# Kernel tuning notes

Measured on AMD Instinct MI355X. Metric: run time of the kernel, lower is better.

## Reference

```python
import jax, jax.numpy as jnp
import numpy as np

B, S, D = 32, 2048, 1024
TEMP = 9.0  # RelaxedBernoulli temperature (torch.tensor([9]))


def setup_inputs() -> dict:
    key = jax.random.key(0)
    ks = jax.random.split(key, 12)
    sd = 1.0 / np.sqrt(D)
    sd2 = 1.0 / np.sqrt(2 * D)
    return {
        "h_t": jax.random.normal(ks[0], (B, D), jnp.float32),
        "h_s": jax.random.normal(ks[1], (B, S, D), jnp.float32),
        "auxi_hs": jax.random.normal(ks[2], (B, S, D), jnp.float32),
        "noise_u": jax.random.uniform(ks[3], (B, S, 1), jnp.float32),
        # linear_map: Linear(2*dim, 1) with bias
        "Wmap": jax.random.normal(ks[4], (2 * D,), jnp.float32) * sd2,
        "bmap": jax.random.normal(ks[5], (), jnp.float32) * sd2,
        # mlp_h: Linear(dim, dim) + Tanh + Linear(dim, 1)
        "W1": jax.random.normal(ks[6], (D, D), jnp.float32) * sd,
        "b1": jax.random.normal(ks[7], (D,), jnp.float32) * sd,
        "W2": jax.random.normal(ks[8], (D,), jnp.float32) * sd,
        "b2": jax.random.normal(ks[9], (), jnp.float32) * sd,
        # linear_out: Linear(2*dim, dim, bias=False) (attn_type='dot')
        "Wout": jax.random.normal(ks[10], (D, 2 * D), jnp.float32) * sd2,
    }


def reference(h_t, h_s, auxi_hs, noise_u, Wmap, bmap, W1, b1, W2, b2, Wout):
    # h_t: (B, D) one-step query; h_s, auxi_hs: (B, S, D)
    d = h_s.shape[-1]
    # linear_map(concat(auxi_hs, H_t)) without materializing the (B,S,2D) concat
    Wm_a, Wm_t = Wmap[:d], Wmap[d:]
    logits_p = jnp.einsum('bsd,d->bs', auxi_hs, Wm_a) + (h_t @ Wm_t)[:, None] + bmap  # (B,S)
    logits_p = logits_p[..., None]  # (B,S,1); note logit(sigmoid(x)) == x
    # RelaxedBernoulli(temp=9, probs=sigmoid(logits_p)).sample() with explicit uniform noise
    eps = 1e-7
    u = jnp.clip(noise_u, eps, 1.0 - eps)
    logistic = jnp.log(u) - jnp.log1p(-u)  # (B,S,1)
    G = jax.nn.sigmoid((logits_p + logistic) / TEMP)  # (B,S,1)
    # mlp_h(h_s): Linear -> tanh -> Linear
    e = jnp.einsum('bsd,d->bs', jnp.tanh(jnp.einsum('bsd,ed->bse', h_s, W1) + b1), W2) + b2
    e = e[..., None]  # (B,S,1)
    # custom softmax: max over dim 0 (batch!), exp, gate
    v = jnp.max(e, axis=0, keepdims=True)  # (1,S,1)
    scores = jnp.exp(e - v) * G  # (B,S,1)
    align = scores[..., 0] / jnp.sum(scores[..., 0], axis=1, keepdims=True)  # (B,S)
    c = jnp.einsum('bs,bsd->bd', align, h_s)  # (B,D)
    attn_h = jnp.tanh(jnp.concatenate([c, h_t], axis=-1) @ Wout.T)  # (B,D)
    return attn_h, align
```

## Files before the change

### kernel.cpp

```cpp
#include <hip/hip_runtime.h>
#include <hip/hip_bf16.h>
#include <math.h>

#define B_ 32
#define S_ 2048
#define D_ 1024
#define TEMP_ 9.0f

typedef __attribute__((ext_vector_type(8))) short short8;
typedef __attribute__((ext_vector_type(4))) float f32x4;
typedef __attribute__((ext_vector_type(4))) unsigned short ushort4v;

__device__ __forceinline__ unsigned short f2b(float f) {
  union { float f; unsigned int u; } v; v.f = f;
  unsigned int r = v.u;
  r += 0x7fffu + ((r >> 16) & 1u);
  return (unsigned short)(r >> 16);
}
__device__ __forceinline__ float b2f(unsigned short b) {
  union { float f; unsigned int u; } v; v.u = ((unsigned int)b) << 16;
  return v.f;
}
__device__ __forceinline__ float tanh_fast(float x) {
  float ez = __expf(2.f * x);
  return 1.f - __fdividef(2.f, ez + 1.f);
}

#define GLOAD_LDS16(g, l) \
  __builtin_amdgcn_global_load_lds((const __attribute__((address_space(1))) void*)(g), \
                                   (__attribute__((address_space(3))) void*)(l), 16, 0, 0)

__global__ void k_conv(const float* __restrict__ src, unsigned short* __restrict__ dst, int n8) {
  int i = blockIdx.x * 256 + threadIdx.x;
  if (i >= n8) return;
  const float4* g = reinterpret_cast<const float4*>(src) + (size_t)i * 2;
  float4 x0 = g[0], x1 = g[1];
  uint4 w;
  w.x = f2b(x0.x) | ((unsigned)f2b(x0.y) << 16);
  w.y = f2b(x0.z) | ((unsigned)f2b(x0.w) << 16);
  w.z = f2b(x1.x) | ((unsigned)f2b(x1.y) << 16);
  w.w = f2b(x1.z) | ((unsigned)f2b(x1.w) << 16);
  reinterpret_cast<uint4*>(dst)[i] = w;
}

__global__ void k_pack_w1(const float* __restrict__ W1, unsigned short* __restrict__ w1t) {
  int c2 = blockIdx.x * 256 + threadIdx.x;
  int l   = c2 & 63;
  int n   = (c2 >> 6) & 7;
  int T   = (c2 >> 9) & 31;
  int rid = c2 >> 14;
  int col = (rid >> 1) * 256 + (rid & 1) * 128 + n * 16 + (l & 15);
  int k0  = T * 32 + (l >> 4) * 8;
  const float* src = W1 + (size_t)col * D_ + k0;
  float4 x0 = *reinterpret_cast<const float4*>(src);
  float4 x1 = *reinterpret_cast<const float4*>(src + 4);
  uint4 w;
  w.x = f2b(x0.x) | ((unsigned)f2b(x0.y) << 16);
  w.y = f2b(x0.z) | ((unsigned)f2b(x0.w) << 16);
  w.z = f2b(x1.x) | ((unsigned)f2b(x1.y) << 16);
  w.w = f2b(x1.z) | ((unsigned)f2b(x1.w) << 16);
  reinterpret_cast<uint4*>(w1t)[c2] = w;
}

__global__ void k0_tdot(const float* __restrict__ h_t, const float* __restrict__ Wmap,
                        const float* __restrict__ bmap, float* __restrict__ tdot) {
  int b = blockIdx.x;
  int t = threadIdx.x;
  float p = 0.f;
  for (int k = t; k < D_; k += 256) p += h_t[b*D_ + k] * Wmap[D_ + k];
  __shared__ float red[256];
  red[t] = p; __syncthreads();
  for (int off = 128; off > 0; off >>= 1) { if (t < off) red[t] += red[t+off]; __syncthreads(); }
  if (t == 0) tdot[b] = red[0] + bmap[0];
}

__global__ void k1_gate(const float* __restrict__ aux, const float* __restrict__ Wmap,
                        const float* __restrict__ noise, const float* __restrict__ tdot,
                        float* __restrict__ Gout) {
  int w = (blockIdx.x * 256 + threadIdx.x) >> 6;
  int lane = threadIdx.x & 63;
  const float4* arow = reinterpret_cast<const float4*>(aux + (size_t)w * D_);
  const float4* wrow = reinterpret_cast<const float4*>(Wmap);
  float p = 0.f;
  for (int it = 0; it < 4; ++it) {
    float4 a = arow[it*64 + lane];
    float4 m = wrow[it*64 + lane];
    p += a.x*m.x + a.y*m.y + a.z*m.z + a.w*m.w;
  }
  for (int msk = 32; msk > 0; msk >>= 1) p += __shfl_xor(p, msk);
  if (lane == 0) {
    int b = w >> 11;
    float logits = p + tdot[b];
    float u = noise[w];
    u = fminf(fmaxf(u, 1e-7f), 1.f - 1e-7f);
    float logistic = logf(u) - log1pf(-u);
    float x = (logits + logistic) / TEMP_;
    Gout[w] = 1.f / (1.f + expf(-x));
  }
}

extern __shared__ unsigned short lds2[];

__global__ __launch_bounds__(256, 2) void k2gt(
    const unsigned short* __restrict__ Ag, const unsigned short* __restrict__ w1t,
    const float* __restrict__ b1, const float* __restrict__ W2,
    float* __restrict__ e_buf,
    const float* __restrict__ aux, const float* __restrict__ Wmap,
    const float* __restrict__ noise, const float* __restrict__ tdot,
    float* __restrict__ Gout) {
  int bid = blockIdx.x;
  int xcd = bid & 7;
  int sub = bid >> 3;
  int cc  = sub & 3;
  int rc  = xcd + 8 * (sub >> 2);
  int rowBase = rc * 128;
  int colBase = cc * 256;

  int t = threadIdx.x;
  int lane = t & 63;
  int wv = t >> 6;
  int wr = wv >> 1, wc = wv & 1;
  int kslot = lane >> 4;

  int aOff[4];
#pragma unroll
  for (int m = 0; m < 4; ++m) {
    int r = wr * 64 + m * 16 + (lane & 15);
    aOff[m] = r * 64 + ((kslot ^ ((r >> 1) & 3)) << 4);
  }

  const unsigned short* gA[2];
  int dstA[2];
#pragma unroll
  for (int i = 0; i < 2; ++i) {
    int c = i * 256 + t;
    int r = c >> 2;
    int clog = (c & 3) ^ ((r >> 1) & 3);
    gA[i] = Ag + (size_t)(rowBase + r) * D_ + clog * 8;
    dstA[i] = c * 16;
  }

  const unsigned short* pBbase = w1t + (size_t)(cc * 2 + wc) * 131072 + lane * 8;

  f32x4 acc[4][8] = {};
  short8 bfA[8], bfB[8];

#define STAGE(TT) do {                                                         \
    char* _ba = (char*)lds2 + ((TT) & 3) * 8192;                               \
    GLOAD_LDS16(gA[0] + (TT) * 32, _ba + dstA[0]);                             \
    GLOAD_LDS16(gA[1] + (TT) * 32, _ba + dstA[1]);                             \
  } while (0)

#define K2_TILE(T, VM, DO_B, DO_S, BFC, BFN) do {                              \
    asm volatile("s_waitcnt lgkmcnt(0)\n\ts_waitcnt vmcnt(" #VM ")" ::: "memory"); \
    __builtin_amdgcn_s_barrier();                                              \
    const char* _ab = (const char*)lds2 + ((T) & 3) * 8192;                    \
    short8 af[4];                                                              \
    _Pragma("unroll")                                                          \
    for (int m = 0; m < 4; ++m)                                                \
      af[m] = *reinterpret_cast<const short8*>(_ab + aOff[m]);                 \
    if (DO_B) {                                                                \
      _Pragma("unroll")                                                        \
      for (int n = 0; n < 8; ++n)                                              \
        BFN[n] = *reinterpret_cast<const short8*>(pBbase + ((T) + 1) * 4096 + n * 512); \
    }                                                                          \
    if (DO_S) STAGE((T) + 3);                                                  \
    __builtin_amdgcn_s_setprio(1);                                             \
    _Pragma("unroll")                                                          \
    for (int m = 0; m < 4; ++m)                                                \
      _Pragma("unroll")                                                        \
      for (int n = 0; n < 8; ++n)                                              \
        acc[m][n] = __builtin_amdgcn_mfma_f32_16x16x32_bf16(af[m], BFC[n], acc[m][n], 0, 0, 0); \
    __builtin_amdgcn_s_setprio(0);                                             \
  } while (0)

  STAGE(0); STAGE(1); STAGE(2);
#pragma unroll
  for (int n = 0; n < 8; ++n)
    bfA[n] = *reinterpret_cast<const short8*>(pBbase + n * 512);

  K2_TILE(0, 0, true, true, bfA, bfB);
#pragma unroll
  for (int tt = 1; tt < 28; tt += 2) {
    K2_TILE(tt,     2, true, true, bfB, bfA);
    K2_TILE(tt + 1, 2, true, true, bfA, bfB);
  }
  K2_TILE(29, 2, true,  false, bfB, bfA);
  K2_TILE(30, 0, true,  false, bfA, bfB);
  K2_TILE(31, 0, false, false, bfB, bfA);
#undef K2_TILE
#undef STAGE

  float b1v[8], w2v[8];
#pragma unroll
  for (int n = 0; n < 8; ++n) {
    int col = colBase + wc * 128 + n * 16 + (lane & 15);
    b1v[n] = b1[col];
    w2v[n] = W2[col];
  }
#pragma unroll
  for (int m = 0; m < 4; ++m) {
#pragma unroll
    for (int j = 0; j < 4; ++j) {
      float s = 0.f;
#pragma unroll
      for (int n = 0; n < 8; ++n)
        s += tanh_fast(acc[m][n][j] + b1v[n]) * w2v[n];
      s += __shfl_xor(s, 1);
      s += __shfl_xor(s, 2);
      s += __shfl_xor(s, 4);
      s += __shfl_xor(s, 8);
      if ((lane & 15) == 0) {
        int row = rowBase + wr * 64 + m * 16 + ((lane >> 4) << 2) + j;
        atomicAdd(&e_buf[row], s);
      }
    }
  }

  {
    const float4* wrow = reinterpret_cast<const float4*>(Wmap);
    float4 m0 = wrow[lane], m1 = wrow[64 + lane], m2 = wrow[128 + lane], m3 = wrow[192 + lane];
    int rowG = (bid << 5) | (wv << 3);
#pragma unroll 2
    for (int i = 0; i < 8; ++i) {
      int row = rowG + i;
      const float4* arow = reinterpret_cast<const float4*>(aux + (size_t)row * D_);
      float4 a0 = arow[lane], a1 = arow[64 + lane], a2 = arow[128 + lane], a3 = arow[192 + lane];
      float p = a0.x*m0.x + a0.y*m0.y + a0.z*m0.z + a0.w*m0.w
              + a1.x*m1.x + a1.y*m1.y + a1.z*m1.z + a1.w*m1.w
              + a2.x*m2.x + a2.y*m2.y + a2.z*m2.z + a2.w*m2.w
              + a3.x*m3.x + a3.y*m3.y + a3.z*m3.z + a3.w*m3.w;
      for (int msk = 32; msk > 0; msk >>= 1) p += __shfl_xor(p, msk);
      if (lane == 0) {
        float logits = p + tdot[row >> 11];
        float u = noise[row];
        u = fminf(fmaxf(u, 1e-7f), 1.f - 1e-7f);
        float logistic = logf(u) - log1pf(-u);
        float x = (logits + logistic) / TEMP_;
        Gout[row] = 1.f / (1.f + expf(-x));
      }
    }
  }
}

#define BM 128
#define BN 128
#define BK 64
__global__ __launch_bounds__(256) void k2_egemm_f32(
    const float* __restrict__ h_s, const float* __restrict__ W1,
    const float* __restrict__ b1, const float* __restrict__ W2,
    float* __restrict__ e_buf) {
  __shared__ unsigned short As[BM * BK];
  __shared__ unsigned short Bs[BN * BK];
  int bid = blockIdx.x;
  int colBase = (bid & 7) * BN;
  int rowBase = (bid >> 3) * BM;
  int t = threadIdx.x;
  int lane = t & 63;
  int wave = t >> 6;
  int wr = wave >> 1, wc = wave & 1;
  f32x4 acc[4][4] = {};
  for (int k0 = 0; k0 < D_; k0 += BK) {
    __syncthreads();
    for (int i = 0; i < 4; ++i) {
      int flat = i*256 + t;
      int r = flat >> 3;
      int c8 = flat & 7;
      int byte = (r*128 + c8*16) ^ ((r & 7) << 4);
      {
        const float4* g = reinterpret_cast<const float4*>(h_s + (size_t)(rowBase + r)*D_ + k0 + c8*8);
        float4 x0 = g[0], x1 = g[1];
        uint4 w;
        w.x = f2b(x0.x) | ((unsigned)f2b(x0.y) << 16);
        w.y = f2b(x0.z) | ((unsigned)f2b(x0.w) << 16);
        w.z = f2b(x1.x) | ((unsigned)f2b(x1.y) << 16);
        w.w = f2b(x1.z) | ((unsigned)f2b(x1.w) << 16);
        *reinterpret_cast<uint4*>(reinterpret_cast<char*>(As) + byte) = w;
      }
      {
        const float4* g = reinterpret_cast<const float4*>(W1 + (size_t)(colBase + r)*D_ + k0 + c8*8);
        float4 x0 = g[0], x1 = g[1];
        uint4 w;
        w.x = f2b(x0.x) | ((unsigned)f2b(x0.y) << 16);
        w.y = f2b(x0.z) | ((unsigned)f2b(x0.w) << 16);
        w.z = f2b(x1.x) | ((unsigned)f2b(x1.y) << 16);
        w.w = f2b(x1.z) | ((unsigned)f2b(x1.w) << 16);
        *reinterpret_cast<uint4*>(reinterpret_cast<char*>(Bs) + byte) = w;
      }
    }
    __syncthreads();
    for (int kk = 0; kk < BK; kk += 32) {
      short8 af[4], bf[4];
      int kByte = kk*2 + ((lane >> 4) << 4);
      for (int m = 0; m < 4; ++m) {
        int r = wr*64 + m*16 + (lane & 15);
        int byte = (r*128 + kByte) ^ ((r & 7) << 4);
        af[m] = *reinterpret_cast<const short8*>(reinterpret_cast<const char*>(As) + byte);
      }
      for (int n = 0; n < 4; ++n) {
        int r = wc*64 + n*16 + (lane & 15);
        int byte = (r*128 + kByte) ^ ((r & 7) << 4);
        bf[n] = *reinterpret_cast<const short8*>(reinterpret_cast<const char*>(Bs) + byte);
      }
      for (int m = 0; m < 4; ++m)
        for (int n = 0; n < 4; ++n)
          acc[m][n] = __builtin_amdgcn_mfma_f32_16x16x32_bf16(af[m], bf[n], acc[m][n], 0, 0, 0);
    }
  }
  float b1v[4], w2v[4];
  for (int n = 0; n < 4; ++n) {
    int col = colBase + wc*64 + n*16 + (lane & 15);
    b1v[n] = b1[col];
    w2v[n] = W2[col];
  }
  for (int m = 0; m < 4; ++m) {
    for (int j = 0; j < 4; ++j) {
      float s = 0.f;
      for (int n = 0; n < 4; ++n)
        s += tanhf(acc[m][n][j] + b1v[n]) * w2v[n];
      s += __shfl_xor(s, 1);
      s += __shfl_xor(s, 2);
      s += __shfl_xor(s, 4);
      s += __shfl_xor(s, 8);
      if ((lane & 15) == 0) {
        int row = rowBase + wr*64 + m*16 + ((lane >> 4) << 2) + j;
        atomicAdd(&e_buf[row], s);
      }
    }
  }
}

__global__ void k3a_vmax(const float* __restrict__ e_buf, float* __restrict__ v) {
  int s = blockIdx.x * 256 + threadIdx.x;
  if (s >= S_) return;
  float m = -1e30f;
  for (int b = 0; b < B_; ++b) m = fmaxf(m, e_buf[b*S_ + s]);
  v[s] = m;
}

__global__ void k3b_align(const float* __restrict__ e_buf, const float* __restrict__ v,
                          float* __restrict__ galign) {
  int b = blockIdx.x;
  int t = threadIdx.x;
  __shared__ float sc[S_];
  __shared__ float red[256];
  float p = 0.f;
  for (int s = t; s < S_; s += 256) {
    float x = expf(e_buf[b*S_ + s] - v[s]) * galign[b*S_ + s];
    sc[s] = x;
    p += x;
  }
  red[t] = p; __syncthreads();
  for (int off = 128; off > 0; off >>= 1) { if (t < off) red[t] += red[t+off]; __syncthreads(); }
  float inv = 1.f / red[0];
  for (int s = t; s < S_; s += 256) galign[b*S_ + s] = sc[s] * inv;
}

__global__ void k4_ctx_bf16(const unsigned short* __restrict__ hsb, const float* __restrict__ align,
                            float* __restrict__ c) {
  int bid = blockIdx.x;
  int b = bid >> 6;
  int sBase = (bid & 63) * 32;
  int t = threadIdx.x;
  float4 accv = {0.f, 0.f, 0.f, 0.f};
  for (int si = 0; si < 32; ++si) {
    int s = sBase + si;
    float a = align[b*S_ + s];
    ushort4v hv = *reinterpret_cast<const ushort4v*>(hsb + (size_t)(b*S_ + s)*D_ + t*4);
    accv.x += a*b2f(hv.x); accv.y += a*b2f(hv.y); accv.z += a*b2f(hv.z); accv.w += a*b2f(hv.w);
  }
  atomicAdd(&c[b*D_ + t*4 + 0], accv.x);
  atomicAdd(&c[b*D_ + t*4 + 1], accv.y);
  atomicAdd(&c[b*D_ + t*4 + 2], accv.z);
  atomicAdd(&c[b*D_ + t*4 + 3], accv.w);
}

__global__ void k4_ctx_f32(const float* __restrict__ h_s, const float* __restrict__ align,
                           float* __restrict__ c) {
  int bid = blockIdx.x;
  int b = bid >> 6;
  int sBase = (bid & 63) * 32;
  int t = threadIdx.x;
  float4 accv = {0.f, 0.f, 0.f, 0.f};
  for (int si = 0; si < 32; ++si) {
    int s = sBase + si;
    float a = align[b*S_ + s];
    float4 hv = *reinterpret_cast<const float4*>(h_s + (size_t)(b*S_ + s)*D_ + t*4);
    accv.x += a*hv.x; accv.y += a*hv.y; accv.z += a*hv.z; accv.w += a*hv.w;
  }
  atomicAdd(&c[b*D_ + t*4 + 0], accv.x);
  atomicAdd(&c[b*D_ + t*4 + 1], accv.y);
  atomicAdd(&c[b*D_ + t*4 + 2], accv.z);
  atomicAdd(&c[b*D_ + t*4 + 3], accv.w);
}

__global__ void k5_out(const float* __restrict__ c, const float* __restrict__ h_t,
                       const float* __restrict__ Wout, float* __restrict__ out) {
  int W = (blockIdx.x * 256 + threadIdx.x) >> 6;
  int lane = threadIdx.x & 63;
  int b = W >> 10;
  int o = W & 1023;
  const float* wrow = Wout + (size_t)o * (2 * D_);
  float p = 0.f;
  for (int it = 0; it < 16; ++it) {
    int k = it*64 + lane;
    p += c[b*D_ + k] * wrow[k];
  }
  for (int it = 16; it < 32; ++it) {
    int k = it*64 + lane;
    p += h_t[b*D_ + (k - D_)] * wrow[k];
  }
  for (int m = 32; m > 0; m >>= 1) p += __shfl_xor(p, m);
  if (lane == 0) out[b*D_ + o] = tanhf(p);
}

extern "C" void kernel_launch(void* const* d_in, const int* in_sizes, int n_in,
                              void* d_out, int out_size, void* d_ws, size_t ws_size,
                              hipStream_t stream) {
  const float* h_t   = (const float*)d_in[0];
  const float* h_s   = (const float*)d_in[1];
  const float* aux   = (const float*)d_in[2];
  const float* noise = (const float*)d_in[3];
  const float* Wmap  = (const float*)d_in[4];
  const float* bmap  = (const float*)d_in[5];
  const float* W1    = (const float*)d_in[6];
  const float* b1    = (const float*)d_in[7];
  const float* W2    = (const float*)d_in[8];
  const float* Wout  = (const float*)d_in[10];

  float* out    = (float*)d_out;
  float* galign = out + B_*D_;

  const size_t HS_N   = (size_t)B_*S_*D_;
  const size_t W1_N   = (size_t)D_*D_;
  const size_t needed = HS_N*2 + W1_N*2 + (65536 + 32 + 2048 + 32768) * sizeof(float);

  if (ws_size >= needed) {
    unsigned short* hs_bf = (unsigned short*)d_ws;
    unsigned short* w1t   = hs_bf + HS_N;
    float* fws   = (float*)(w1t + W1_N);
    float* e_buf = fws;
    float* tdot  = fws + 65536;
    float* v     = fws + 65568;
    float* c     = fws + 67616;

    hipMemsetAsync(e_buf, 0, 65536 * sizeof(float), stream);
    hipMemsetAsync(c, 0, 32768 * sizeof(float), stream);

    hipFuncSetAttribute(reinterpret_cast<const void*>(k2gt),
                        hipFuncAttributeMaxDynamicSharedMemorySize, 32768);

    k_conv<<<(int)(HS_N/8/256), 256, 0, stream>>>(h_s, hs_bf, (int)(HS_N/8));
    k_pack_w1<<<512, 256, 0, stream>>>(W1, w1t);
    k0_tdot<<<32, 256, 0, stream>>>(h_t, Wmap, bmap, tdot);
    k2gt<<<2048, 256, 32768, stream>>>(hs_bf, w1t, b1, W2, e_buf,
                                       aux, Wmap, noise, tdot, galign);
    k3a_vmax<<<8, 256, 0, stream>>>(e_buf, v);
    k3b_align<<<32, 256, 0, stream>>>(e_buf, v, galign);
    k4_ctx_bf16<<<2048, 256, 0, stream>>>(hs_bf, galign, c);
    k5_out<<<8192, 256, 0, stream>>>(c, h_t, Wout, out);
  } else {
    float* ws    = (float*)d_ws;
    float* e_buf = ws;
    float* tdot  = ws + 65536;
    float* v     = ws + 65568;
    float* c     = ws + 67616;

    hipMemsetAsync(e_buf, 0, 65536 * sizeof(float), stream);
    hipMemsetAsync(c, 0, 32768 * sizeof(float), stream);

    k0_tdot<<<32, 256, 0, stream>>>(h_t, Wmap, bmap, tdot);
    k1_gate<<<16384, 256, 0, stream>>>(aux, Wmap, noise, tdot, galign);
    k2_egemm_f32<<<4096, 256, 0, stream>>>(h_s, W1, b1, W2, e_buf);
    k3a_vmax<<<8, 256, 0, stream>>>(e_buf, v);
    k3b_align<<<32, 256, 0, stream>>>(e_buf, v, galign);
    k4_ctx_f32<<<2048, 256, 0, stream>>>(h_s, galign, c);
    k5_out<<<8192, 256, 0, stream>>>(c, h_t, Wout, out);
  }
}
```

Baseline: 350.0 us.

## Fuse h_s fp32-to-bf16 conversion into GEMM tile loads, drop separate conversion pass

```diff
diff --git a/kernel.cpp b/kernel.cpp
--- a/kernel.cpp
+++ b/kernel.cpp
@@ -21,6 +21,11 @@
   union { float f; unsigned int u; } v; v.u = ((unsigned int)b) << 16;
   return v.f;
 }
+__device__ __forceinline__ unsigned cvtpk(float a, float b) {
+  unsigned r;
+  asm("v_cvt_pk_bf16_f32 %0, %1, %2" : "=v"(r) : "v"(a), "v"(b));
+  return r;
+}
 __device__ __forceinline__ float tanh_fast(float x) {
   float ez = __expf(2.f * x);
   return 1.f - __fdividef(2.f, ez + 1.f);
@@ -29,19 +34,6 @@
 #define GLOAD_LDS16(g, l) \
   __builtin_amdgcn_global_load_lds((const __attribute__((address_space(1))) void*)(g), \
                                    (__attribute__((address_space(3))) void*)(l), 16, 0, 0)
-
-__global__ void k_conv(const float* __restrict__ src, unsigned short* __restrict__ dst, int n8) {
-  int i = blockIdx.x * 256 + threadIdx.x;
-  if (i >= n8) return;
-  const float4* g = reinterpret_cast<const float4*>(src) + (size_t)i * 2;
-  float4 x0 = g[0], x1 = g[1];
-  uint4 w;
-  w.x = f2b(x0.x) | ((unsigned)f2b(x0.y) << 16);
-  w.y = f2b(x0.z) | ((unsigned)f2b(x0.w) << 16);
-  w.z = f2b(x1.x) | ((unsigned)f2b(x1.y) << 16);
-  w.w = f2b(x1.z) | ((unsigned)f2b(x1.w) << 16);
-  reinterpret_cast<uint4*>(dst)[i] = w;
-}
 
 __global__ void k_pack_w1(const float* __restrict__ W1, unsigned short* __restrict__ w1t) {
   int c2 = blockIdx.x * 256 + threadIdx.x;
@@ -101,8 +93,8 @@
 
 extern __shared__ unsigned short lds2[];
 
-__global__ __launch_bounds__(256, 2) void k2gt(
-    const unsigned short* __restrict__ Ag, const unsigned short* __restrict__ w1t,
+__global__ __launch_bounds__(256, 2) void k2f(
+    const float* __restrict__ h_s, const unsigned short* __restrict__ w1t,
     const float* __restrict__ b1, const float* __restrict__ W2,
     float* __restrict__ e_buf,
     const float* __restrict__ aux, const float* __restrict__ Wmap,
@@ -122,21 +114,22 @@
   int wr = wv >> 1, wc = wv & 1;
   int kslot = lane >> 4;
 
-  int aOff[4];
+  int aOff0[4], aOff1[4];
 #pragma unroll
   for (int m = 0; m < 4; ++m) {
     int r = wr * 64 + m * 16 + (lane & 15);
-    aOff[m] = r * 64 + ((kslot ^ ((r >> 1) & 3)) << 4);
-  }
-
-  const unsigned short* gA[2];
-  int dstA[2];
-#pragma unroll
-  for (int i = 0; i < 2; ++i) {
+    aOff0[m] = r * 128 + (((2 * kslot)     ^ (r & 7)) << 4);
+    aOff1[m] = r * 128 + (((2 * kslot + 1) ^ (r & 7)) << 4);
+  }
+
+  const float* gA[4];
+  int dstA[4];
+#pragma unroll
+  for (int i = 0; i < 4; ++i) {
     int c = i * 256 + t;
-    int r = c >> 2;
-    int clog = (c & 3) ^ ((r >> 1) & 3);
-    gA[i] = Ag + (size_t)(rowBase + r) * D_ + clog * 8;
+    int r = c >> 3;
+    int lg = (c & 7) ^ (r & 7);
+    gA[i] = h_s + (size_t)(rowBase + r) * D_ + lg * 4;
     dstA[i] = c * 16;
   }
 
@@ -146,25 +139,39 @@
   short8 bfA[8], bfB[8];
 
 #define STAGE(TT) do {                                                         \
-    char* _ba = (char*)lds2 + ((TT) & 3) * 8192;                               \
+    char* _ba = (char*)lds2 + ((TT) & 3) * 16384;                              \
     GLOAD_LDS16(gA[0] + (TT) * 32, _ba + dstA[0]);                             \
     GLOAD_LDS16(gA[1] + (TT) * 32, _ba + dstA[1]);                             \
+    GLOAD_LDS16(gA[2] + (TT) * 32, _ba + dstA[2]);                             \
+    GLOAD_LDS16(gA[3] + (TT) * 32, _ba + dstA[3]);                             \
   } while (0)
 
 #define K2_TILE(T, VM, DO_B, DO_S, BFC, BFN) do {                              \
     asm volatile("s_waitcnt lgkmcnt(0)\n\ts_waitcnt vmcnt(" #VM ")" ::: "memory"); \
     __builtin_amdgcn_s_barrier();                                              \
-    const char* _ab = (const char*)lds2 + ((T) & 3) * 8192;                    \
-    short8 af[4];                                                              \
+    const char* _ab = (const char*)lds2 + ((T) & 3) * 16384;                   \
+    f32x4 lo[4], hi[4];                                                        \
     _Pragma("unroll")                                                          \
-    for (int m = 0; m < 4; ++m)                                                \
-      af[m] = *reinterpret_cast<const short8*>(_ab + aOff[m]);                 \
+    for (int m = 0; m < 4; ++m) {                                              \
+      lo[m] = *reinterpret_cast<const f32x4*>(_ab + aOff0[m]);                 \
+      hi[m] = *reinterpret_cast<const f32x4*>(_ab + aOff1[m]);                 \
+    }                                                                          \
     if (DO_B) {                                                                \
       _Pragma("unroll")                                                        \
       for (int n = 0; n < 8; ++n)                                              \
         BFN[n] = *reinterpret_cast<const short8*>(pBbase + ((T) + 1) * 4096 + n * 512); \
     }                                                                          \
     if (DO_S) STAGE((T) + 3);                                                  \
+    short8 af[4];                                                              \
+    _Pragma("unroll")                                                          \
+    for (int m = 0; m < 4; ++m) {                                              \
+      union { unsigned u[4]; short8 s; } cv;                                   \
+      cv.u[0] = cvtpk(lo[m][0], lo[m][1]);                                     \
+      cv.u[1] = cvtpk(lo[m][2], lo[m][3]);                                     \
+      cv.u[2] = cvtpk(hi[m][0], hi[m][1]);                                     \
+      cv.u[3] = cvtpk(hi[m][2], hi[m][3]);                                     \
+      af[m] = cv.s;                                                            \
+    }                                                                          \
     __builtin_amdgcn_s_setprio(1);                                             \
     _Pragma("unroll")                                                          \
     for (int m = 0; m < 4; ++m)                                                \
@@ -181,11 +188,11 @@
 
   K2_TILE(0, 0, true, true, bfA, bfB);
 #pragma unroll
-  for (int tt = 1; tt < 28; tt += 2) {
-    K2_TILE(tt,     2, true, true, bfB, bfA);
-    K2_TILE(tt + 1, 2, true, true, bfA, bfB);
-  }
-  K2_TILE(29, 2, true,  false, bfB, bfA);
+  for (int tt = 1; tt < 29; tt += 2) {
+    K2_TILE(tt,     4, true, true, bfB, bfA);
+    K2_TILE(tt + 1, 4, true, true, bfA, bfB);
+  }
+  K2_TILE(29, 4, true,  false, bfB, bfA);
   K2_TILE(30, 0, true,  false, bfA, bfB);
   K2_TILE(31, 0, false, false, bfB, bfA);
 #undef K2_TILE
@@ -356,25 +363,6 @@
   for (int s = t; s < S_; s += 256) galign[b*S_ + s] = sc[s] * inv;
 }
 
-__global__ void k4_ctx_bf16(const unsigned short* __restrict__ hsb, const float* __restrict__ align,
-                            float* __restrict__ c) {
-  int bid = blockIdx.x;
-  int b = bid >> 6;
-  int sBase = (bid & 63) * 32;
-  int t = threadIdx.x;
-  float4 accv = {0.f, 0.f, 0.f, 0.f};
-  for (int si = 0; si < 32; ++si) {
-    int s = sBase + si;
-    float a = align[b*S_ + s];
-    ushort4v hv = *reinterpret_cast<const ushort4v*>(hsb + (size_t)(b*S_ + s)*D_ + t*4);
-    accv.x += a*b2f(hv.x); accv.y += a*b2f(hv.y); accv.z += a*b2f(hv.z); accv.w += a*b2f(hv.w);
-  }
-  atomicAdd(&c[b*D_ + t*4 + 0], accv.x);
-  atomicAdd(&c[b*D_ + t*4 + 1], accv.y);
-  atomicAdd(&c[b*D_ + t*4 + 2], accv.z);
-  atomicAdd(&c[b*D_ + t*4 + 3], accv.w);
-}
-
 __global__ void k4_ctx_f32(const float* __restrict__ h_s, const float* __restrict__ align,
                            float* __restrict__ c) {
   int bid = blockIdx.x;
@@ -431,13 +419,11 @@
   float* out    = (float*)d_out;
   float* galign = out + B_*D_;
 
-  const size_t HS_N   = (size_t)B_*S_*D_;
   const size_t W1_N   = (size_t)D_*D_;
-  const size_t needed = HS_N*2 + W1_N*2 + (65536 + 32 + 2048 + 32768) * sizeof(float);
+  const size_t needed = W1_N*2 + (65536 + 32 + 2048 + 32768) * sizeof(float);
 
   if (ws_size >= needed) {
-    unsigned short* hs_bf = (unsigned short*)d_ws;
-    unsigned short* w1t   = hs_bf + HS_N;
+    unsigned short* w1t = (unsigned short*)d_ws;
     float* fws   = (float*)(w1t + W1_N);
     float* e_buf = fws;
     float* tdot  = fws + 65536;
@@ -447,17 +433,16 @@
     hipMemsetAsync(e_buf, 0, 65536 * sizeof(float), stream);
     hipMemsetAsync(c, 0, 32768 * sizeof(float), stream);
 
-    hipFuncSetAttribute(reinterpret_cast<const void*>(k2gt),
-                        hipFuncAttributeMaxDynamicSharedMemorySize, 32768);
-
-    k_conv<<<(int)(HS_N/8/256), 256, 0, stream>>>(h_s, hs_bf, (int)(HS_N/8));
+    hipFuncSetAttribute(reinterpret_cast<const void*>(k2f),
+                        hipFuncAttributeMaxDynamicSharedMemorySize, 65536);
+
     k_pack_w1<<<512, 256, 0, stream>>>(W1, w1t);
     k0_tdot<<<32, 256, 0, stream>>>(h_t, Wmap, bmap, tdot);
-    k2gt<<<2048, 256, 32768, stream>>>(hs_bf, w1t, b1, W2, e_buf,
-                                       aux, Wmap, noise, tdot, galign);
+    k2f<<<2048, 256, 65536, stream>>>(h_s, w1t, b1, W2, e_buf,
+                                      aux, Wmap, noise, tdot, galign);
     k3a_vmax<<<8, 256, 0, stream>>>(e_buf, v);
     k3b_align<<<32, 256, 0, stream>>>(e_buf, v, galign);
-    k4_ctx_bf16<<<2048, 256, 0, stream>>>(hs_bf, galign, c);
+    k4_ctx_f32<<<2048, 256, 0, stream>>>(h_s, galign, c);
     k5_out<<<8192, 256, 0, stream>>>(c, h_t, Wout, out);
   } else {
     float* ws    = (float*)d_ws;
```

Measured after the change: 360.8 us. 3.1% more time.
